# Kernel optimization log

Hardware: AMD Instinct MI355X
Metric: run time of the kernel (lower is better)

The kernel has to match this reference:

```python
import jax, jax.numpy as jnp
import numpy as np

N = 50000       # nodes
D = 256         # in_features == out_features
G = 4           # feature groups / adjacencies
E = 800000      # edges per group (avg degree 16)


def setup_inputs() -> dict:
    key = jax.random.key(0)
    k1, k2, k3, k4, k5, k6 = jax.random.split(key, 6)
    x = jax.random.normal(k1, (N, D), dtype=jnp.float32)
    edge_row = jax.random.randint(k2, (G, E), 0, N, dtype=jnp.int32)
    edge_col = jax.random.randint(k3, (G, E), 0, N, dtype=jnp.int32)
    edge_val = jax.random.uniform(k4, (G, E), dtype=jnp.float32)
    stdv = 1.0 / np.sqrt(D)
    weight = jax.random.normal(k5, (D, D), dtype=jnp.float32) * stdv
    bias = jax.random.normal(k6, (D,), dtype=jnp.float32) * stdv
    return {"x": x, "edge_row": edge_row, "edge_col": edge_col,
            "edge_val": edge_val, "weight": weight, "bias": bias}


def reference(x, edge_row, edge_col, edge_val, weight, bias):
    n, d = x.shape
    g = edge_row.shape[0]
    dg = d // g
    # [G, N, dg]: contiguous column blocks per group
    xg = x.reshape(n, g, dg).transpose(1, 0, 2)

    def spmm(xb, row, col, val):
        # out[r] += val * xb[c]  (reduce='add' SpMM)
        msg = val[:, None] * xb[col]          # [E, dg]
        return jax.ops.segment_sum(msg, row, num_segments=n)

    outs = jax.vmap(spmm)(xg, edge_row, edge_col, edge_val)  # [G, N, dg]
    outputs = outs.transpose(1, 0, 2).reshape(n, d)           # [N, D]
    return outputs @ weight + bias
```

## Files before the change

### kernel.cpp

```cpp
#include <hip/hip_runtime.h>
#include <hip/hip_bf16.h>

#define N_NODES 50000
#define D_FEAT  256
#define G_GROUPS 4
#define E_EDGES 800000
#define DG      64
#define M_SEG   (G_GROUPS * N_NODES)
#define TOT_E   (G_GROUPS * E_EDGES)
#define M_PAD   50048

#define SEGB      512
#define NB1       391
#define CA_BLOCKS 400
#define CHA       8000
#define CHG       (CHA / 4)
#define PADMAX    512

typedef short bf16x8 __attribute__((ext_vector_type(8)));
typedef float f32x4  __attribute__((ext_vector_type(4)));

__device__ __forceinline__ unsigned short f2bf(float f) {
    unsigned int u = __float_as_uint(f);
    u += 0x7FFF + ((u >> 16) & 1);
    return (unsigned short)(u >> 16);
}
__device__ __forceinline__ float bf2f(unsigned short h) {
    return __uint_as_float((unsigned int)h << 16);
}

__global__ __launch_bounds__(256) void convert_x_kernel(
    const float* __restrict__ x, unsigned short* __restrict__ xb)
{
    const long long base = ((long long)blockIdx.x * 256 + threadIdx.x) * 8;
    if (base >= (long long)N_NODES * D_FEAT) return;
    const float4 v0 = *(const float4*)&x[base];
    const float4 v1 = *(const float4*)&x[base + 4];
    unsigned short r[8];
    r[0] = f2bf(v0.x); r[1] = f2bf(v0.y); r[2] = f2bf(v0.z); r[3] = f2bf(v0.w);
    r[4] = f2bf(v1.x); r[5] = f2bf(v1.y); r[6] = f2bf(v1.z); r[7] = f2bf(v1.w);
    *(uint4*)&xb[base] = *(const uint4*)r;
}

__global__ __launch_bounds__(256) void convert_w_kernel(
    const float* __restrict__ W, unsigned short* __restrict__ Wt)
{
    const int n = blockIdx.x;
    const int k = threadIdx.x;
    Wt[n * D_FEAT + k] = f2bf(W[k * D_FEAT + n]);
}

__global__ __launch_bounds__(1024) void countA_kernel(
    const int* __restrict__ edge_row, int* __restrict__ cntA)
{
    __shared__ int h[NB1];
    const int t = threadIdx.x;
    if (t < NB1) h[t] = 0;
    __syncthreads();
    const int start = blockIdx.x * CHA;
    const int segbase = (start / E_EDGES) * N_NODES;
    for (int gi = t; gi < CHG; gi += 1024) {
        const int4 r = *(const int4*)&edge_row[start + gi * 4];
        atomicAdd(&h[(segbase + r.x) >> 9], 1);
        atomicAdd(&h[(segbase + r.y) >> 9], 1);
        atomicAdd(&h[(segbase + r.z) >> 9], 1);
        atomicAdd(&h[(segbase + r.w) >> 9], 1);
    }
    __syncthreads();
    if (t < NB1 && h[t]) atomicAdd(&cntA[t], h[t]);
}

__global__ __launch_bounds__(256) void scanA_kernel(
    const int* __restrict__ cntA, int* __restrict__ ofsA, int* __restrict__ curA)
{
    __shared__ int ssum[256];
    const int t = threadIdx.x;
    const int i0 = 2 * t, i1 = 2 * t + 1;
    const int v0 = (i0 < NB1) ? cntA[i0] : 0;
    const int v1 = (i1 < NB1) ? cntA[i1] : 0;
    ssum[t] = v0 + v1;
    __syncthreads();
    for (int off = 1; off < 256; off <<= 1) {
        const int add = (t >= off) ? ssum[t - off] : 0;
        __syncthreads();
        ssum[t] += add;
        __syncthreads();
    }
    const int eb = ssum[t] - (v0 + v1);
    if (i0 < NB1) { ofsA[i0] = eb;      curA[i0] = eb; }
    if (i1 < NB1) { ofsA[i1] = eb + v0; curA[i1] = eb + v0; }
    if (t == 255) ofsA[NB1] = ssum[255];
}

__global__ __launch_bounds__(1024) void scatterA_kernel(
    const int* __restrict__ edge_row, const int* __restrict__ edge_col,
    const float* __restrict__ edge_val, int* __restrict__ curA,
    int2* __restrict__ epA)
{
    __shared__ int hist[NB1];
    __shared__ int gcur[NB1];
    const int t = threadIdx.x;
    if (t < NB1) hist[t] = 0;
    __syncthreads();
    const int start = blockIdx.x * CHA;
    const int segbase = (start / E_EDGES) * N_NODES;
    const bool hasB = (t + 1024) < CHG;

    const int4 ra = *(const int4*)&edge_row[start + 4 * t];
    int4 rb = make_int4(0, 0, 0, 0);
    if (hasB) rb = *(const int4*)&edge_row[start + 4 * (t + 1024)];
    const int sA0 = segbase + ra.x, sA1 = segbase + ra.y;
    const int sA2 = segbase + ra.z, sA3 = segbase + ra.w;
    atomicAdd(&hist[sA0 >> 9], 1);
    atomicAdd(&hist[sA1 >> 9], 1);
    atomicAdd(&hist[sA2 >> 9], 1);
    atomicAdd(&hist[sA3 >> 9], 1);
    int sB0 = 0, sB1 = 0, sB2 = 0, sB3 = 0;
    if (hasB) {
        sB0 = segbase + rb.x; sB1 = segbase + rb.y;
        sB2 = segbase + rb.z; sB3 = segbase + rb.w;
        atomicAdd(&hist[sB0 >> 9], 1);
        atomicAdd(&hist[sB1 >> 9], 1);
        atomicAdd(&hist[sB2 >> 9], 1);
        atomicAdd(&hist[sB3 >> 9], 1);
    }
    __syncthreads();
    if (t < NB1) gcur[t] = hist[t] ? atomicAdd(&curA[t], hist[t]) : 0;
    __syncthreads();
    {
        const int4 c = *(const int4*)&edge_col[start + 4 * t];
        const int4 v = *(const int4*)&((const int*)edge_val)[start + 4 * t];
        int pos;
        pos = atomicAdd(&gcur[sA0 >> 9], 1);
        epA[pos] = make_int2(c.x | ((sA0 & (SEGB - 1)) << 16), v.x);
        pos = atomicAdd(&gcur[sA1 >> 9], 1);
        epA[pos] = make_int2(c.y | ((sA1 & (SEGB - 1)) << 16), v.y);
        pos = atomicAdd(&gcur[sA2 >> 9], 1);
        epA[pos] = make_int2(c.z | ((sA2 & (SEGB - 1)) << 16), v.z);
        pos = atomicAdd(&gcur[sA3 >> 9], 1);
        epA[pos] = make_int2(c.w | ((sA3 & (SEGB - 1)) << 16), v.w);
    }
    if (hasB) {
        const int4 c = *(const int4*)&edge_col[start + 4 * (t + 1024)];
        const int4 v = *(const int4*)&((const int*)edge_val)[start + 4 * (t + 1024)];
        int pos;
        pos = atomicAdd(&gcur[sB0 >> 9], 1);
        epA[pos] = make_int2(c.x | ((sB0 & (SEGB - 1)) << 16), v.x);
        pos = atomicAdd(&gcur[sB1 >> 9], 1);
        epA[pos] = make_int2(c.y | ((sB1 & (SEGB - 1)) << 16), v.y);
        pos = atomicAdd(&gcur[sB2 >> 9], 1);
        epA[pos] = make_int2(c.z | ((sB2 & (SEGB - 1)) << 16), v.z);
        pos = atomicAdd(&gcur[sB3 >> 9], 1);
        epA[pos] = make_int2(c.w | ((sB3 & (SEGB - 1)) << 16), v.w);
    }
}

__global__ __launch_bounds__(512) void sortB_kernel(
    const int2* __restrict__ epA, const int* __restrict__ ofsA,
    int2* __restrict__ epB, unsigned* __restrict__ ofs)
{
    __shared__ int hist[SEGB];
    __shared__ int lofs[SEGB];
    __shared__ int cur[SEGB];
    __shared__ int ssum[256];
    const int b = blockIdx.x;
    const int t = threadIdx.x;
    const int s = ofsA[b], e = ofsA[b + 1];
    const int base = s + b * PADMAX;
    hist[t] = 0;
    __syncthreads();
    for (int j = s + t; j < e; j += 512)
        atomicAdd(&hist[((unsigned)epA[j].x) >> 16], 1);
    __syncthreads();
    int p0 = 0, p1 = 0, sum = 0;
    if (t < 256) {
        const int c0 = hist[2 * t], c1 = hist[2 * t + 1];
        p0 = c0 + (c0 & 1); p1 = c1 + (c1 & 1);
        sum = p0 + p1;
        ssum[t] = sum;
    }
    __syncthreads();
    for (int off = 1; off < 256; off <<= 1) {
        int add = 0;
        if (t < 256 && t >= off) add = ssum[t - off];
        __syncthreads();
        if (t < 256) ssum[t] += add;
        __syncthreads();
    }
    if (t < 256) {
        const int eb = ssum[t] - sum;
        lofs[2 * t]     = eb;      cur[2 * t]     = eb;
        lofs[2 * t + 1] = eb + p0; cur[2 * t + 1] = eb + p0;
    }
    __syncthreads();
    const int seg0 = b * SEGB;
    const int nseg = min(SEGB, M_SEG - seg0);
    if (t < nseg) {
        const int pc = hist[t] + (hist[t] & 1);
        ofs[seg0 + t] = (unsigned)(base + lofs[t]) | ((unsigned)pc << 24);
    }
    for (int j = s + t; j < e; j += 512) {
        const int2 p = epA[j];
        const int sl = ((unsigned)p.x) >> 16;
        const int col = p.x & 0xFFFF;
        const int seg = seg0 + sl;
        const int g = seg / N_NODES;
        const int pos = atomicAdd(&cur[sl], 1);
        epB[base + pos] = make_int2((col << 9) | (g << 7), p.y);
    }
    if (t < nseg && (hist[t] & 1))
        epB[base + lofs[t] + hist[t]] = make_int2(0, 0);
}

__global__ __launch_bounds__(256) void spmm_csr_kernel(
    const unsigned short* __restrict__ xb, const int2* __restrict__ ep,
    const unsigned* __restrict__ ofs, unsigned short* __restrict__ tmpb)
{
    const int w   = (blockIdx.x * 256 + threadIdx.x) >> 6;
    const int tl  = threadIdx.x & 63;
    const int o   = tl >> 3;
    const int ls  = tl & 7;
    const int seg = w * 8 + o;
    const int g   = seg / N_NODES;
    const int row = seg - g * N_NODES;

    const char* __restrict__ xbb = (const char*)xb + ls * 16;

    const unsigned po = ofs[seg];
    int j       = (int)(po & 0xFFFFFFu);
    const int e = j + (int)(po >> 24);
    const int emax2 = (e - 2 < j) ? j : (e - 2);

    float a0 = 0.f, a1 = 0.f, a2 = 0.f, a3 = 0.f;
    float a4 = 0.f, a5 = 0.f, a6 = 0.f, a7 = 0.f;

#define ACC8(v, r)                                          \
    a0 = fmaf(v, __uint_as_float((r).x << 16), a0);         \
    a1 = fmaf(v, __uint_as_float((r).x & 0xFFFF0000u), a1); \
    a2 = fmaf(v, __uint_as_float((r).y << 16), a2);         \
    a3 = fmaf(v, __uint_as_float((r).y & 0xFFFF0000u), a3); \
    a4 = fmaf(v, __uint_as_float((r).z << 16), a4);         \
    a5 = fmaf(v, __uint_as_float((r).z & 0xFFFF0000u), a5); \
    a6 = fmaf(v, __uint_as_float((r).w << 16), a6);         \
    a7 = fmaf(v, __uint_as_float((r).w & 0xFFFF0000u), a7);

    while (__ballot(j < e)) {
        const int jc0 = min(j, emax2);
        const int jc1 = min(j + 2, emax2);
        const int4 q0 = *(const int4*)&ep[jc0];
        const int4 q1 = *(const int4*)&ep[jc1];
        const bool cA = j < e;
        const bool cB = (j + 2) < e;
        const int o0 = cA ? q0.x : 0;
        const int o1 = cA ? q0.z : 0;
        const int o2 = cB ? q1.x : 0;
        const int o3 = cB ? q1.z : 0;
        const uint4 r0 = *(const uint4*)(xbb + o0);
        const uint4 r1 = *(const uint4*)(xbb + o1);
        const uint4 r2 = *(const uint4*)(xbb + o2);
        const uint4 r3 = *(const uint4*)(xbb + o3);
        const float v0 = cA ? __int_as_float(q0.y) : 0.f;
        const float v1 = cA ? __int_as_float(q0.w) : 0.f;
        const float v2 = cB ? __int_as_float(q1.y) : 0.f;
        const float v3 = cB ? __int_as_float(q1.w) : 0.f;
        ACC8(v0, r0)
        ACC8(v1, r1)
        ACC8(v2, r2)
        ACC8(v3, r3)
        j += 4;
    }
#undef ACC8

    const unsigned o0w = (unsigned)f2bf(a0) | ((unsigned)f2bf(a1) << 16);
    const unsigned o1w = (unsigned)f2bf(a2) | ((unsigned)f2bf(a3) << 16);
    const unsigned o2w = (unsigned)f2bf(a4) | ((unsigned)f2bf(a5) << 16);
    const unsigned o3w = (unsigned)f2bf(a6) | ((unsigned)f2bf(a7) << 16);
    *(uint4*)((char*)tmpb + (size_t)row * 512 + g * 128 + ls * 16) =
        make_uint4(o0w, o1w, o2w, o3w);
}

#define TBK 32
#define LDP 40

__global__ __launch_bounds__(256) void gemm_mfma_kernel(
    const unsigned short* __restrict__ A, const unsigned short* __restrict__ Bt,
    const float* __restrict__ bias, float* __restrict__ C)
{
    __shared__ unsigned short As[128][LDP];
    __shared__ unsigned short Bs[128][LDP];

    const int tid = threadIdx.x;
    const int wid = tid >> 6, lane = tid & 63;
    const int wm = (wid & 1) * 64, wn = (wid >> 1) * 64;
    const int lm = lane & 15, lq = lane >> 4;
    const int row0 = blockIdx.x * 128, col0 = blockIdx.y * 128;

    f32x4 acc[4][4] = {};

    for (int k0 = 0; k0 < D_FEAT; k0 += TBK) {
        #pragma unroll
        for (int l = 0; l < 2; ++l) {
            const int chunk = tid + l * 256;
            const int r = chunk >> 2;
            const int c = (chunk & 3) * 8;
            uint4 v = make_uint4(0u, 0u, 0u, 0u);
            const int gr = row0 + r;
            if (gr < N_NODES)
                v = *(const uint4*)&A[(long long)gr * D_FEAT + k0 + c];
            *(uint4*)&As[r][c] = v;
        }
        #pragma unroll
        for (int l = 0; l < 2; ++l) {
            const int chunk = tid + l * 256;
            const int r = chunk >> 2;
            const int c = (chunk & 3) * 8;
            *(uint4*)&Bs[r][c] =
                *(const uint4*)&Bt[(long long)(col0 + r) * D_FEAT + k0 + c];
        }
        __syncthreads();

        bf16x8 af[4], bfr[4];
        #pragma unroll
        for (int mi = 0; mi < 4; ++mi)
            af[mi] = *(const bf16x8*)&As[wm + mi * 16 + lm][lq * 8];
        #pragma unroll
        for (int ni = 0; ni < 4; ++ni)
            bfr[ni] = *(const bf16x8*)&Bs[wn + ni * 16 + lm][lq * 8];
        #pragma unroll
        for (int mi = 0; mi < 4; ++mi)
            #pragma unroll
            for (int ni = 0; ni < 4; ++ni)
                acc[mi][ni] = __builtin_amdgcn_mfma_f32_16x16x32_bf16(
                    af[mi], bfr[ni], acc[mi][ni], 0, 0, 0);
        __syncthreads();
    }

    #pragma unroll
    for (int mi = 0; mi < 4; ++mi) {
        #pragma unroll
        for (int ni = 0; ni < 4; ++ni) {
            const int n = col0 + wn + ni * 16 + lm;
            const float b = bias[n];
            #pragma unroll
            for (int r = 0; r < 4; ++r) {
                const int m = row0 + wm + mi * 16 + lq * 4 + r;
                if (m < N_NODES)
                    C[(long long)m * D_FEAT + n] = acc[mi][ni][r] + b;
            }
        }
    }
}

__global__ __launch_bounds__(256) void spmm_scatter_kernel(
    const float* __restrict__ x, const int* __restrict__ edge_row,
    const int* __restrict__ edge_col, const float* __restrict__ edge_val,
    float* __restrict__ tmp)
{
    const long long gtid = (long long)blockIdx.x * blockDim.x + threadIdx.x;
    const int wave = (int)(gtid >> 6);
    const int lane = threadIdx.x & 63;
    if (wave >= TOT_E) return;
    const int g = wave / E_EDGES;
    const int row = edge_row[wave];
    const int col = edge_col[wave];
    const float val = edge_val[wave];
    atomicAdd(&tmp[(long long)row * D_FEAT + g * DG + lane],
              val * x[(long long)col * D_FEAT + g * DG + lane]);
}

__global__ __launch_bounds__(256) void gemm_bias_kernel(
    const float* __restrict__ A, const float* __restrict__ W,
    const float* __restrict__ bias, float* __restrict__ C)
{
    __shared__ float Asf[64][68];
    __shared__ float Wsf[64][68];
    const int tid = threadIdx.x;
    const int tx = tid & 15, ty = tid >> 4;
    const int row0 = blockIdx.x * 64, col0 = blockIdx.y * 64;
    float acc[4][4] = {};
    for (int k0 = 0; k0 < D_FEAT; k0 += 64) {
        #pragma unroll
        for (int l = 0; l < 4; ++l) {
            const int linear = tid + l * 256;
            const int ar = linear >> 4, ac = (linear & 15) << 2;
            float4 v = make_float4(0.f, 0.f, 0.f, 0.f);
            const int gr = row0 + ar;
            if (gr < N_NODES) v = *(const float4*)&A[(long long)gr * D_FEAT + k0 + ac];
            Asf[ac + 0][ar] = v.x; Asf[ac + 1][ar] = v.y;
            Asf[ac + 2][ar] = v.z; Asf[ac + 3][ar] = v.w;
        }
        #pragma unroll
        for (int l = 0; l < 4; ++l) {
            const int linear = tid + l * 256;
            const int wr = linear >> 4, wc = (linear & 15) << 2;
            *(float4*)&Wsf[wr][wc] =
                *(const float4*)&W[(long long)(k0 + wr) * D_FEAT + col0 + wc];
        }
        __syncthreads();
        #pragma unroll
        for (int k = 0; k < 64; ++k) {
            const float4 a4 = *(const float4*)&Asf[k][ty * 4];
            const float4 b4 = *(const float4*)&Wsf[k][tx * 4];
            const float a[4] = {a4.x, a4.y, a4.z, a4.w};
            const float b[4] = {b4.x, b4.y, b4.z, b4.w};
            #pragma unroll
            for (int i = 0; i < 4; ++i)
                #pragma unroll
                for (int j = 0; j < 4; ++j) acc[i][j] += a[i] * b[j];
        }
        __syncthreads();
    }
    const float4 b4 = *(const float4*)&bias[col0 + tx * 4];
    #pragma unroll
    for (int i = 0; i < 4; ++i) {
        const int gr = row0 + ty * 4 + i;
        if (gr >= N_NODES) continue;
        float4 v;
        v.x = acc[i][0] + b4.x; v.y = acc[i][1] + b4.y;
        v.z = acc[i][2] + b4.z; v.w = acc[i][3] + b4.w;
        *(float4*)&C[(long long)gr * D_FEAT + col0 + tx * 4] = v;
    }
}

extern "C" void kernel_launch(void* const* d_in, const int* in_sizes, int n_in,
                              void* d_out, int out_size, void* d_ws, size_t ws_size,
                              hipStream_t stream)
{
    const float* x        = (const float*)d_in[0];
    const int*   edge_row = (const int*)d_in[1];
    const int*   edge_col = (const int*)d_in[2];
    const float* edge_val = (const float*)d_in[3];
    const float* weight   = (const float*)d_in[4];
    const float* bias     = (const float*)d_in[5];
    float* out = (float*)d_out;

    char* p = (char*)d_ws;
    auto alloc = [&](size_t bytes) {
        char* r = p;
        p += (bytes + 255) & ~(size_t)255;
        return r;
    };
    unsigned short* xb   = (unsigned short*)alloc((size_t)N_NODES * D_FEAT * 2);
    unsigned short* tmpb = (unsigned short*)alloc((size_t)M_PAD * D_FEAT * 2);
    unsigned short* Wt   = (unsigned short*)alloc((size_t)D_FEAT * D_FEAT * 2);
    int2* epB = (int2*)alloc(((size_t)TOT_E + (size_t)NB1 * PADMAX + 8)
                             * sizeof(int2));
    int* cntA = (int*)alloc((size_t)NB1 * sizeof(int));
    int* ofsA = (int*)alloc((size_t)(NB1 + 1) * sizeof(int));
    int* curA = (int*)alloc((size_t)NB1 * sizeof(int));
    unsigned* ofs = (unsigned*)alloc((size_t)M_SEG * sizeof(unsigned));
    const size_t needed = (size_t)(p - (char*)d_ws);

    int2* epA = (int2*)tmpb;

    if (ws_size >= needed) {
        hipMemsetAsync(cntA, 0, (size_t)NB1 * sizeof(int), stream);
        convert_x_kernel<<<(N_NODES * D_FEAT / 8 + 255) / 256, 256, 0, stream>>>(x, xb);
        convert_w_kernel<<<D_FEAT, D_FEAT, 0, stream>>>(weight, Wt);
        countA_kernel<<<CA_BLOCKS, 1024, 0, stream>>>(edge_row, cntA);
        scanA_kernel<<<1, 256, 0, stream>>>(cntA, ofsA, curA);
        scatterA_kernel<<<CA_BLOCKS, 1024, 0, stream>>>(
            edge_row, edge_col, edge_val, curA, epA);
        sortB_kernel<<<NB1, 512, 0, stream>>>(epA, ofsA, epB, ofs);
        spmm_csr_kernel<<<(M_SEG / 8) * 64 / 256, 256, 0, stream>>>(xb, epB, ofs, tmpb);
        dim3 grid(M_PAD / 128, D_FEAT / 128);
        gemm_mfma_kernel<<<grid, 256, 0, stream>>>(tmpb, Wt, bias, out);
    } else {
        float* tmp = (float*)d_ws;
        hipMemsetAsync(tmp, 0, (size_t)N_NODES * D_FEAT * sizeof(float), stream);
        const long long total_threads = (long long)TOT_E * 64;
        spmm_scatter_kernel<<<(int)((total_threads + 255) / 256), 256, 0, stream>>>(
            x, edge_row, edge_col, edge_val, tmp);
        dim3 grid2((N_NODES + 63) / 64, D_FEAT / 64);
        gemm_bias_kernel<<<grid2, 256, 0, stream>>>(tmp, weight, bias, out);
    }
}
```

Baseline: 293.3 us.

## Fuse prep kernels, halve sort bucket size, pad segments to 4 for 8-wide SpMM unroll

Merges the x/W bf16 conversions and the row-count histogram into one launch, which removes several kernel launches. It halves the bucket size to 256 segments per block, doubling the number of sortB blocks. Each segment's edges are padded to a multiple of 4 and the gaps between buckets are zero-filled. This lets the SpMM loop read 8 edges per iteration without clamping, raising memory-level parallelism for the gathers. The cost is more padding writes and extra zero edges to process.

```diff
diff --git a/kernel.cpp b/kernel.cpp
--- a/kernel.cpp
+++ b/kernel.cpp
@@ -10,12 +10,16 @@
 #define TOT_E   (G_GROUPS * E_EDGES)
 #define M_PAD   50048
 
-#define SEGB      512
-#define NB1       391
+#define SEGB      256
+#define NB1       782
 #define CA_BLOCKS 400
 #define CHA       8000
 #define CHG       (CHA / 4)
-#define PADMAX    512
+#define PADMAX    770
+
+#define PREP_CVX  1563
+#define PREP_CW   64
+#define PREP_TOT  (PREP_CVX + PREP_CW + CA_BLOCKS)
 
 typedef short bf16x8 __attribute__((ext_vector_type(8)));
 typedef float f32x4  __attribute__((ext_vector_type(4)));
@@ -29,67 +33,64 @@
     return __uint_as_float((unsigned int)h << 16);
 }
 
-__global__ __launch_bounds__(256) void convert_x_kernel(
-    const float* __restrict__ x, unsigned short* __restrict__ xb)
-{
-    const long long base = ((long long)blockIdx.x * 256 + threadIdx.x) * 8;
-    if (base >= (long long)N_NODES * D_FEAT) return;
-    const float4 v0 = *(const float4*)&x[base];
-    const float4 v1 = *(const float4*)&x[base + 4];
-    unsigned short r[8];
-    r[0] = f2bf(v0.x); r[1] = f2bf(v0.y); r[2] = f2bf(v0.z); r[3] = f2bf(v0.w);
-    r[4] = f2bf(v1.x); r[5] = f2bf(v1.y); r[6] = f2bf(v1.z); r[7] = f2bf(v1.w);
-    *(uint4*)&xb[base] = *(const uint4*)r;
-}
-
-__global__ __launch_bounds__(256) void convert_w_kernel(
-    const float* __restrict__ W, unsigned short* __restrict__ Wt)
-{
-    const int n = blockIdx.x;
-    const int k = threadIdx.x;
-    Wt[n * D_FEAT + k] = f2bf(W[k * D_FEAT + n]);
-}
-
-__global__ __launch_bounds__(1024) void countA_kernel(
+__global__ __launch_bounds__(1024) void prep_kernel(
+    const float* __restrict__ x, unsigned short* __restrict__ xb,
+    const float* __restrict__ W, unsigned short* __restrict__ Wt,
     const int* __restrict__ edge_row, int* __restrict__ cntA)
 {
     __shared__ int h[NB1];
-    const int t = threadIdx.x;
+    const int b = blockIdx.x, t = threadIdx.x;
+
+    if (b < PREP_CVX) {
+        const long long base = ((long long)b * 1024 + t) * 8;
+        if (base < (long long)N_NODES * D_FEAT) {
+            const float4 v0 = *(const float4*)&x[base];
+            const float4 v1 = *(const float4*)&x[base + 4];
+            unsigned short r[8];
+            r[0] = f2bf(v0.x); r[1] = f2bf(v0.y); r[2] = f2bf(v0.z); r[3] = f2bf(v0.w);
+            r[4] = f2bf(v1.x); r[5] = f2bf(v1.y); r[6] = f2bf(v1.z); r[7] = f2bf(v1.w);
+            *(uint4*)&xb[base] = *(const uint4*)r;
+        }
+        return;
+    }
+    if (b < PREP_CVX + PREP_CW) {
+        const int idx = (b - PREP_CVX) * 1024 + t;
+        const int n = idx >> 8, k = idx & 255;
+        Wt[n * D_FEAT + k] = f2bf(W[k * D_FEAT + n]);
+        return;
+    }
+    const int cb = b - PREP_CVX - PREP_CW;
     if (t < NB1) h[t] = 0;
     __syncthreads();
-    const int start = blockIdx.x * CHA;
+    const int start = cb * CHA;
     const int segbase = (start / E_EDGES) * N_NODES;
     for (int gi = t; gi < CHG; gi += 1024) {
         const int4 r = *(const int4*)&edge_row[start + gi * 4];
-        atomicAdd(&h[(segbase + r.x) >> 9], 1);
-        atomicAdd(&h[(segbase + r.y) >> 9], 1);
-        atomicAdd(&h[(segbase + r.z) >> 9], 1);
-        atomicAdd(&h[(segbase + r.w) >> 9], 1);
+        atomicAdd(&h[(segbase + r.x) >> 8], 1);
+        atomicAdd(&h[(segbase + r.y) >> 8], 1);
+        atomicAdd(&h[(segbase + r.z) >> 8], 1);
+        atomicAdd(&h[(segbase + r.w) >> 8], 1);
     }
     __syncthreads();
     if (t < NB1 && h[t]) atomicAdd(&cntA[t], h[t]);
 }
 
-__global__ __launch_bounds__(256) void scanA_kernel(
+__global__ __launch_bounds__(1024) void scanA_kernel(
     const int* __restrict__ cntA, int* __restrict__ ofsA, int* __restrict__ curA)
 {
-    __shared__ int ssum[256];
+    __shared__ int ssum[1024];
     const int t = threadIdx.x;
-    const int i0 = 2 * t, i1 = 2 * t + 1;
-    const int v0 = (i0 < NB1) ? cntA[i0] : 0;
-    const int v1 = (i1 < NB1) ? cntA[i1] : 0;
-    ssum[t] = v0 + v1;
-    __syncthreads();
-    for (int off = 1; off < 256; off <<= 1) {
+    const int v = (t < NB1) ? cntA[t] : 0;
+    ssum[t] = v;
+    __syncthreads();
+    for (int off = 1; off < 1024; off <<= 1) {
         const int add = (t >= off) ? ssum[t - off] : 0;
         __syncthreads();
         ssum[t] += add;
         __syncthreads();
     }
-    const int eb = ssum[t] - (v0 + v1);
-    if (i0 < NB1) { ofsA[i0] = eb;      curA[i0] = eb; }
-    if (i1 < NB1) { ofsA[i1] = eb + v0; curA[i1] = eb + v0; }
-    if (t == 255) ofsA[NB1] = ssum[255];
+    if (t < NB1) { ofsA[t] = ssum[t] - v; curA[t] = ssum[t] - v; }
+    if (t == 1023) ofsA[NB1] = ssum[1023];
 }
 
 __global__ __launch_bounds__(1024) void scatterA_kernel(
@@ -111,18 +112,18 @@
     if (hasB) rb = *(const int4*)&edge_row[start + 4 * (t + 1024)];
     const int sA0 = segbase + ra.x, sA1 = segbase + ra.y;
     const int sA2 = segbase + ra.z, sA3 = segbase + ra.w;
-    atomicAdd(&hist[sA0 >> 9], 1);
-    atomicAdd(&hist[sA1 >> 9], 1);
-    atomicAdd(&hist[sA2 >> 9], 1);
-    atomicAdd(&hist[sA3 >> 9], 1);
+    atomicAdd(&hist[sA0 >> 8], 1);
+    atomicAdd(&hist[sA1 >> 8], 1);
+    atomicAdd(&hist[sA2 >> 8], 1);
+    atomicAdd(&hist[sA3 >> 8], 1);
     int sB0 = 0, sB1 = 0, sB2 = 0, sB3 = 0;
     if (hasB) {
         sB0 = segbase + rb.x; sB1 = segbase + rb.y;
         sB2 = segbase + rb.z; sB3 = segbase + rb.w;
-        atomicAdd(&hist[sB0 >> 9], 1);
-        atomicAdd(&hist[sB1 >> 9], 1);
-        atomicAdd(&hist[sB2 >> 9], 1);
-        atomicAdd(&hist[sB3 >> 9], 1);
+        atomicAdd(&hist[sB0 >> 8], 1);
+        atomicAdd(&hist[sB1 >> 8], 1);
+        atomicAdd(&hist[sB2 >> 8], 1);
+        atomicAdd(&hist[sB3 >> 8], 1);
     }
     __syncthreads();
     if (t < NB1) gcur[t] = hist[t] ? atomicAdd(&curA[t], hist[t]) : 0;
@@ -131,26 +132,26 @@
         const int4 c = *(const int4*)&edge_col[start + 4 * t];
         const int4 v = *(const int4*)&((const int*)edge_val)[start + 4 * t];
         int pos;
-        pos = atomicAdd(&gcur[sA0 >> 9], 1);
+        pos = atomicAdd(&gcur[sA0 >> 8], 1);
         epA[pos] = make_int2(c.x | ((sA0 & (SEGB - 1)) << 16), v.x);
-        pos = atomicAdd(&gcur[sA1 >> 9], 1);
+        pos = atomicAdd(&gcur[sA1 >> 8], 1);
         epA[pos] = make_int2(c.y | ((sA1 & (SEGB - 1)) << 16), v.y);
-        pos = atomicAdd(&gcur[sA2 >> 9], 1);
+        pos = atomicAdd(&gcur[sA2 >> 8], 1);
         epA[pos] = make_int2(c.z | ((sA2 & (SEGB - 1)) << 16), v.z);
-        pos = atomicAdd(&gcur[sA3 >> 9], 1);
+        pos = atomicAdd(&gcur[sA3 >> 8], 1);
         epA[pos] = make_int2(c.w | ((sA3 & (SEGB - 1)) << 16), v.w);
     }
     if (hasB) {
         const int4 c = *(const int4*)&edge_col[start + 4 * (t + 1024)];
         const int4 v = *(const int4*)&((const int*)edge_val)[start + 4 * (t + 1024)];
         int pos;
-        pos = atomicAdd(&gcur[sB0 >> 9], 1);
+        pos = atomicAdd(&gcur[sB0 >> 8], 1);
         epA[pos] = make_int2(c.x | ((sB0 & (SEGB - 1)) << 16), v.x);
-        pos = atomicAdd(&gcur[sB1 >> 9], 1);
+        pos = atomicAdd(&gcur[sB1 >> 8], 1);
         epA[pos] = make_int2(c.y | ((sB1 & (SEGB - 1)) << 16), v.y);
-        pos = atomicAdd(&gcur[sB2 >> 9], 1);
+        pos = atomicAdd(&gcur[sB2 >> 8], 1);
         epA[pos] = make_int2(c.z | ((sB2 & (SEGB - 1)) << 16), v.z);
-        pos = atomicAdd(&gcur[sB3 >> 9], 1);
+        pos = atomicAdd(&gcur[sB3 >> 8], 1);
         epA[pos] = make_int2(c.w | ((sB3 & (SEGB - 1)) << 16), v.w);
     }
 }
@@ -162,54 +163,55 @@
     __shared__ int hist[SEGB];
     __shared__ int lofs[SEGB];
     __shared__ int cur[SEGB];
-    __shared__ int ssum[256];
+    __shared__ int ssum[SEGB];
+    __shared__ int shUsed;
     const int b = blockIdx.x;
     const int t = threadIdx.x;
     const int s = ofsA[b], e = ofsA[b + 1];
-    const int base = s + b * PADMAX;
-    hist[t] = 0;
+    const int rbase = s + b * PADMAX;
+    const int base  = rbase + (rbase & 1);
+    const int nrb   = e + (b + 1) * PADMAX;
+    const int nbase = nrb + (nrb & 1);
+    if (t < SEGB) hist[t] = 0;
     __syncthreads();
     for (int j = s + t; j < e; j += 512)
         atomicAdd(&hist[((unsigned)epA[j].x) >> 16], 1);
     __syncthreads();
-    int p0 = 0, p1 = 0, sum = 0;
-    if (t < 256) {
-        const int c0 = hist[2 * t], c1 = hist[2 * t + 1];
-        p0 = c0 + (c0 & 1); p1 = c1 + (c1 & 1);
-        sum = p0 + p1;
-        ssum[t] = sum;
-    }
-    __syncthreads();
-    for (int off = 1; off < 256; off <<= 1) {
+    int pc = 0;
+    if (t < SEGB) { const int c = hist[t]; pc = (c + 3) & ~3; ssum[t] = pc; }
+    __syncthreads();
+    for (int off = 1; off < SEGB; off <<= 1) {
         int add = 0;
-        if (t < 256 && t >= off) add = ssum[t - off];
-        __syncthreads();
-        if (t < 256) ssum[t] += add;
-        __syncthreads();
-    }
-    if (t < 256) {
-        const int eb = ssum[t] - sum;
-        lofs[2 * t]     = eb;      cur[2 * t]     = eb;
-        lofs[2 * t + 1] = eb + p0; cur[2 * t + 1] = eb + p0;
-    }
+        if (t < SEGB && t >= off) add = ssum[t - off];
+        __syncthreads();
+        if (t < SEGB) ssum[t] += add;
+        __syncthreads();
+    }
+    if (t < SEGB) { const int eb = ssum[t] - pc; lofs[t] = eb; cur[t] = eb; }
+    if (t == SEGB - 1) shUsed = ssum[SEGB - 1];
     __syncthreads();
     const int seg0 = b * SEGB;
     const int nseg = min(SEGB, M_SEG - seg0);
-    if (t < nseg) {
-        const int pc = hist[t] + (hist[t] & 1);
+    if (t < nseg)
         ofs[seg0 + t] = (unsigned)(base + lofs[t]) | ((unsigned)pc << 24);
-    }
     for (int j = s + t; j < e; j += 512) {
         const int2 p = epA[j];
         const int sl = ((unsigned)p.x) >> 16;
         const int col = p.x & 0xFFFF;
-        const int seg = seg0 + sl;
-        const int g = seg / N_NODES;
+        const int gg = (seg0 + sl) / N_NODES;
         const int pos = atomicAdd(&cur[sl], 1);
-        epB[base + pos] = make_int2((col << 9) | (g << 7), p.y);
-    }
-    if (t < nseg && (hist[t] & 1))
-        epB[base + lofs[t] + hist[t]] = make_int2(0, 0);
+        epB[base + pos] = make_int2((col << 9) | (gg << 7), p.y);
+    }
+    if (t < SEGB) {
+        const int c = hist[t];
+        for (int k = c; k < pc; ++k)
+            epB[base + lofs[t] + k] = make_int2(0, 0);
+    }
+    const int used = shUsed;
+    for (int k = base + used + t; k < nbase; k += 512)
+        epB[k] = make_int2(0, 0);
+    if (b == NB1 - 1 && t < 64)
+        epB[nbase + t] = make_int2(0, 0);
 }
 
 __global__ __launch_bounds__(256) void spmm_csr_kernel(
@@ -229,7 +231,6 @@
     const unsigned po = ofs[seg];
     int j       = (int)(po & 0xFFFFFFu);
     const int e = j + (int)(po >> 24);
-    const int emax2 = (e - 2 < j) ? j : (e - 2);
 
     float a0 = 0.f, a1 = 0.f, a2 = 0.f, a3 = 0.f;
     float a4 = 0.f, a5 = 0.f, a6 = 0.f, a7 = 0.f;
@@ -245,29 +246,37 @@
     a7 = fmaf(v, __uint_as_float((r).w & 0xFFFF0000u), a7);
 
     while (__ballot(j < e)) {
-        const int jc0 = min(j, emax2);
-        const int jc1 = min(j + 2, emax2);
-        const int4 q0 = *(const int4*)&ep[jc0];
-        const int4 q1 = *(const int4*)&ep[jc1];
+        const int4 q0 = *(const int4*)&ep[j];
+        const int4 q1 = *(const int4*)&ep[j + 2];
+        const int4 q2 = *(const int4*)&ep[j + 4];
+        const int4 q3 = *(const int4*)&ep[j + 6];
+        const uint4 r0 = *(const uint4*)(xbb + q0.x);
+        const uint4 r1 = *(const uint4*)(xbb + q0.z);
+        const uint4 r2 = *(const uint4*)(xbb + q1.x);
+        const uint4 r3 = *(const uint4*)(xbb + q1.z);
+        const uint4 r4 = *(const uint4*)(xbb + q2.x);
+        const uint4 r5 = *(const uint4*)(xbb + q2.z);
+        const uint4 r6 = *(const uint4*)(xbb + q3.x);
+        const uint4 r7 = *(const uint4*)(xbb + q3.z);
         const bool cA = j < e;
-        const bool cB = (j + 2) < e;
-        const int o0 = cA ? q0.x : 0;
-        const int o1 = cA ? q0.z : 0;
-        const int o2 = cB ? q1.x : 0;
-        const int o3 = cB ? q1.z : 0;
-        const uint4 r0 = *(const uint4*)(xbb + o0);
-        const uint4 r1 = *(const uint4*)(xbb + o1);
-        const uint4 r2 = *(const uint4*)(xbb + o2);
-        const uint4 r3 = *(const uint4*)(xbb + o3);
+        const bool cB = (j + 4) < e;
         const float v0 = cA ? __int_as_float(q0.y) : 0.f;
         const float v1 = cA ? __int_as_float(q0.w) : 0.f;
-        const float v2 = cB ? __int_as_float(q1.y) : 0.f;
-        const float v3 = cB ? __int_as_float(q1.w) : 0.f;
+        const float v2 = cA ? __int_as_float(q1.y) : 0.f;
+        const float v3 = cA ? __int_as_float(q1.w) : 0.f;
+        const float v4 = cB ? __int_as_float(q2.y) : 0.f;
+        const float v5 = cB ? __int_as_float(q2.w) : 0.f;
+        const float v6 = cB ? __int_as_float(q3.y) : 0.f;
+        const float v7 = cB ? __int_as_float(q3.w) : 0.f;
         ACC8(v0, r0)
         ACC8(v1, r1)
         ACC8(v2, r2)
         ACC8(v3, r3)
-        j += 4;
+        ACC8(v4, r4)
+        ACC8(v5, r5)
+        ACC8(v6, r6)
+        ACC8(v7, r7)
+        j += 8;
     }
 #undef ACC8
 
@@ -443,7 +452,7 @@
     unsigned short* xb   = (unsigned short*)alloc((size_t)N_NODES * D_FEAT * 2);
     unsigned short* tmpb = (unsigned short*)alloc((size_t)M_PAD * D_FEAT * 2);
     unsigned short* Wt   = (unsigned short*)alloc((size_t)D_FEAT * D_FEAT * 2);
-    int2* epB = (int2*)alloc(((size_t)TOT_E + (size_t)NB1 * PADMAX + 8)
+    int2* epB = (int2*)alloc(((size_t)TOT_E + (size_t)NB1 * PADMAX + 80)
                              * sizeof(int2));
     int* cntA = (int*)alloc((size_t)NB1 * sizeof(int));
     int* ofsA = (int*)alloc((size_t)(NB1 + 1) * sizeof(int));
@@ -455,10 +464,9 @@
 
     if (ws_size >= needed) {
         hipMemsetAsync(cntA, 0, (size_t)NB1 * sizeof(int), stream);
-        convert_x_kernel<<<(N_NODES * D_FEAT / 8 + 255) / 256, 256, 0, stream>>>(x, xb);
-        convert_w_kernel<<<D_FEAT, D_FEAT, 0, stream>>>(weight, Wt);
-        countA_kernel<<<CA_BLOCKS, 1024, 0, stream>>>(edge_row, cntA);
-        scanA_kernel<<<1, 256, 0, stream>>>(cntA, ofsA, curA);
+        prep_kernel<<<PREP_TOT, 1024, 0, stream>>>(x, xb, weight, Wt,
+                                                   edge_row, cntA);
+        scanA_kernel<<<1, 1024, 0, stream>>>(cntA, ofsA, curA);
         scatterA_kernel<<<CA_BLOCKS, 1024, 0, stream>>>(
             edge_row, edge_col, edge_val, curA, epA);
         sortB_kernel<<<NB1, 512, 0, stream>>>(epA, ofsA, epB, ofs);
```

Result: no change. 295.9 us (+0.9%).
